# Kernel tuning notes

Measured on AMD Instinct MI355X. Metric: run time of the kernel, lower is better.

Reference implementation:

```python
import jax, jax.numpy as jnp
import numpy as np

# Graph sizes hard-coded in the original forward
N_NODE, N_EDGE, N_HEDGE, N_HNODE = 200, 100, 39, 23
LINK_LEN = 3
DIM_IN, DIM_E_IN, DIM_OUT, EMBED_DIM = 64, 16, 128, 10
TIME_DIM = 55
BATCH = 512


def _bigraph_conv(x, edge_index, n_src, n_tgt, W_self, W_agg):
    """Bipartite mean message passing src->tgt->src, mode='cat'.
    x: (b, n_src, c). edge_index: (2, E) int, row0 in [0,n_src), row1 in [0,n_tgt).
    Returns (b, n_src, c_self + c_agg)."""
    src, tgt = edge_index[0], edge_index[1]
    b, _, c = x.shape
    # mean-aggregate node features onto hyperedges
    e_sum = jnp.zeros((b, n_tgt, c), x.dtype).at[:, tgt, :].add(x[:, src, :])
    e_cnt = jnp.zeros((n_tgt,), x.dtype).at[tgt].add(1.0)
    h_e = e_sum / jnp.maximum(e_cnt, 1.0)[None, :, None]
    # mean-aggregate hyperedge features back onto nodes
    n_sum = jnp.zeros((b, n_src, c), x.dtype).at[:, src, :].add(h_e[:, tgt, :])
    n_cnt = jnp.zeros((n_src,), x.dtype).at[src].add(1.0)
    h_n = n_sum / jnp.maximum(n_cnt, 1.0)[None, :, None]
    return jnp.concatenate([x @ W_self, h_n @ W_agg], axis=-1)


def setup_inputs() -> dict:
    key = jax.random.key(0)
    ks = jax.random.split(key, 20)
    f = jnp.float32
    inp = {
        "x": jax.random.normal(ks[0], (BATCH, N_NODE, DIM_IN), f),
        "x_e": jax.random.normal(ks[1], (BATCH, N_EDGE, DIM_E_IN), f),
        "x_time": jax.random.normal(ks[2], (BATCH, 1, TIME_DIM), f),
        "x_window": jax.random.normal(ks[3], (BATCH, N_NODE, 12), f),
        "node_embeddings": jax.random.normal(ks[4], (N_NODE, EMBED_DIM), f),
        "hodge_laplacian": jax.random.normal(ks[5], (N_EDGE, N_EDGE), f) * 0.1,
        "incidence_matrix": jax.random.uniform(ks[6], (N_NODE, N_EDGE), f),
        "hyper_edge_data": jnp.stack([
            jax.random.randint(ks[7], (800,), 0, N_NODE),
            jax.random.randint(ks[8], (800,), 0, N_HEDGE)]).astype(jnp.int32),
        "hyper_node_data": jnp.stack([
            jax.random.randint(ks[9], (400,), 0, N_EDGE),
            jax.random.randint(ks[10], (400,), 0, N_HNODE)]).astype(jnp.int32),
        # learned parameters
        "weights_pool": jax.random.normal(ks[11], (EMBED_DIM, LINK_LEN, DIM_IN + TIME_DIM, DIM_OUT // 2), f) * 0.1,
        "bias_pool": jax.random.normal(ks[12], (EMBED_DIM, DIM_OUT), f) * 0.1,
        "W_node_self": jax.random.normal(ks[13], (DIM_IN, DIM_OUT // 8), f) * 0.1,
        "W_node_agg": jax.random.normal(ks[14], (DIM_IN, DIM_OUT // 8), f) * 0.1,
        "W_edge_self": jax.random.normal(ks[15], (DIM_E_IN, DIM_OUT // 16), f) * 0.1,
        "W_edge_agg": jax.random.normal(ks[16], (DIM_E_IN, DIM_OUT // 16), f) * 0.1,
        "W_hoc": jax.random.normal(ks[17], (DIM_OUT // 8, DIM_OUT // 8), f) * 0.1,
        "b_hoc": jnp.zeros((DIM_OUT // 8,), f),
    }
    return inp


def reference(x, x_e, x_time, x_window, node_embeddings, hodge_laplacian,
              incidence_matrix, hyper_edge_data, hyper_node_data,
              weights_pool, bias_pool, W_node_self, W_node_agg,
              W_edge_self, W_edge_agg, W_hoc, b_hoc):
    n = node_embeddings.shape[0]
    # adaptive support: softmax(relu(E E^T)) and Chebyshev-like powers
    sup = jax.nn.softmax(jax.nn.relu(node_embeddings @ node_embeddings.T), axis=1)
    support_set = [jnp.eye(n, dtype=x.dtype), sup]
    for k in range(2, LINK_LEN):
        support_set.append(sup @ support_set[k - 1])
    supports = jnp.stack(support_set, axis=0)                      # (K, n, n)
    # merge time features: (b,1,55) broadcast to (b,n,55)
    x_time_rep = jnp.broadcast_to(x_time, (x.shape[0], x.shape[1], x_time.shape[2]))
    merge_x = jnp.concatenate([x, x_time_rep], axis=-1)            # (b, n, i)
    # per-node dynamic weights / bias
    weights = jnp.einsum('nd,dkio->nkio', node_embeddings, weights_pool)
    bias = node_embeddings @ bias_pool                             # (n, dim_out)
    # graph conv with dynamic weights
    x_g = jnp.einsum('knm,bmc->bnkc', supports, merge_x)           # (b, n, K, i)
    x_gconv = jnp.einsum('bnki,nkio->bno', x_g, weights)           # (b, n, dim_out/2)
    # hypergraph bipartite convs (dropout is identity in eval mode)
    x_node_hyper = _bigraph_conv(x, hyper_edge_data, N_NODE, N_HEDGE, W_node_self, W_node_agg)
    x_edge_hyper = _bigraph_conv(x_e, hyper_node_data, N_EDGE, N_HNODE, W_edge_self, W_edge_agg)
    # hodge-laplacian higher-order conv on edge features
    x_e_hconv = jnp.einsum('mn,bnc->bmc', hodge_laplacian, x_edge_hyper) @ W_hoc + b_hoc
    x_e_hh = jnp.concatenate([x_edge_hyper, x_e_hconv], axis=-1)   # (b, m, dim_out/4)
    # push edge features onto nodes via incidence matrix
    x_edge_hh_node = jnp.einsum('bmo,nm->bno', x_e_hh, incidence_matrix)
    out = jnp.concatenate([x_gconv, x_node_hyper, x_edge_hh_node], axis=-1) + bias
    return out
```

## Files before the change

kernel.cpp:

```cpp
#include <hip/hip_runtime.h>

typedef unsigned short u16;
typedef unsigned int   u32;
typedef __attribute__((ext_vector_type(8))) short short8;
typedef __attribute__((ext_vector_type(4))) short short4v;
typedef __attribute__((ext_vector_type(4))) float f32x4;

#define OFF_SUP       0
#define OFF_SUP2T     40000
#define OFF_BIAS      80000
#define OFF_RCPHE     105600
#define OFF_RCPN      105664
#define OFF_RCPHN     105920
#define OFF_RCPE      105984
#define OFF_A1        106112
#define OFF_A1E       113912
#define OFF_WNODE     116212
#define OFF_WEDGE     118260
#define OFF_WHOC      118516
#define OFF_BHOC      118772
#define OFF_WECOMB    118788
#define OFF_M3        119556
#define OFF_AN16      139556
#define OFF_AE16      159556
#define OFF_SUPB      164556
#define OFF_G12       234444
#define OFF_G34       257740
#define OFF_WNSB      281036
#define OFF_WNAB      281548
#define OFF_WFF       282060

__device__ __forceinline__ float us2f(u16 u){
  union { float f; u32 i; } v; v.i = ((u32)u) << 16; return v.f;
}
__device__ __forceinline__ u16 f2us(float f){
  u32 u = __float_as_uint(f);
  u += 0x7FFF + ((u >> 16) & 1);
  return (u16)(u >> 16);
}

__global__ __launch_bounds__(256) void k_pre1(
    const float* __restrict__ E, const float* __restrict__ biasP,
    const float* __restrict__ Wns, const float* __restrict__ Wna,
    const float* __restrict__ Wes, const float* __restrict__ Wea,
    const float* __restrict__ Whoc, const float* __restrict__ bhoc,
    const int* __restrict__ hed, const int* __restrict__ hnd,
    float* __restrict__ ws)
{
  const int n = blockIdx.x, t = threadIdx.x;
  __shared__ float Ef[2000];
  __shared__ float arow[200];
  __shared__ float red[256];
  __shared__ int A1i[7800];
  __shared__ int A1ei[2300];
  for (int i=t;i<2000;i+=256) Ef[i] = E[i];
  __syncthreads();
  const float* En = &Ef[n*10];
  for (int m=t;m<200;m+=256){
    float s=0.f;
    #pragma unroll
    for (int d=0;d<10;d++) s += En[d]*Ef[m*10+d];
    arow[m] = fmaxf(s,0.f);
  }
  __syncthreads();
  float mv = -1e30f;
  for (int m=t;m<200;m+=256) mv = fmaxf(mv, arow[m]);
  red[t]=mv; __syncthreads();
  for (int s=128;s>0;s>>=1){ if(t<s) red[t]=fmaxf(red[t],red[t+s]); __syncthreads(); }
  mv = red[0]; __syncthreads();
  float sv=0.f;
  for (int m=t;m<200;m+=256) sv += __expf(arow[m]-mv);
  red[t]=sv; __syncthreads();
  for (int s=128;s>0;s>>=1){ if(t<s) red[t]+=red[t+s]; __syncthreads(); }
  const float inv = 1.f/red[0];
  for (int m=t;m<200;m+=256)
    ws[OFF_SUP + n*200+m] = __expf(arow[m]-mv)*inv;
  for (int o=t;o<128;o+=256){
    float acc=0.f;
    #pragma unroll
    for (int d=0;d<10;d++) acc += En[d]*biasP[d*128+o];
    ws[OFF_BIAS + n*128+o]=acc;
  }
  if (n==0){
    for (int i=t;i<7800;i+=256) A1i[i]=0;
    for (int i=t;i<2300;i+=256) A1ei[i]=0;
    __syncthreads();
    for (int e=t;e<800;e+=256) atomicAdd(&A1i[hed[800+e]*200 + hed[e]], 1);
    for (int e=t;e<400;e+=256) atomicAdd(&A1ei[hnd[400+e]*100 + hnd[e]], 1);
    __syncthreads();
    for (int i=t;i<7800;i+=256) ws[OFF_A1+i]=(float)A1i[i];
    for (int i=t;i<2300;i+=256) ws[OFF_A1E+i]=(float)A1ei[i];
    for (int h=t;h<39;h+=256){ int s=0; for(int m=0;m<200;m++) s+=A1i[h*200+m]; ws[OFF_RCPHE+h]=1.f/fmaxf((float)s,1.f); }
    for (int m=t;m<200;m+=256){ int s=0; for(int h=0;h<39;h++) s+=A1i[h*200+m]; ws[OFF_RCPN+m]=1.f/fmaxf((float)s,1.f); }
    for (int h=t;h<23;h+=256){ int s=0; for(int m=0;m<100;m++) s+=A1ei[h*100+m]; ws[OFF_RCPHN+h]=1.f/fmaxf((float)s,1.f); }
    for (int m=t;m<100;m+=256){ int s=0; for(int h=0;h<23;h++) s+=A1ei[h*100+m]; ws[OFF_RCPE+m]=1.f/fmaxf((float)s,1.f); }
  }
  if (n==1){
    for (int idx=t;idx<2048;idx+=256){ int j=idx>>5,c=idx&31;
      ws[OFF_WNODE+idx]= (c<16? Wns[j*16+c] : Wna[j*16+(c-16)]); }
    { int j=t>>4, c=t&15;
      ws[OFF_WEDGE+t]= (c<8? Wes[j*8+c] : Wea[j*8+(c-8)]);
      ws[OFF_WHOC+t]= Whoc[t]; }
    if (t<16) ws[OFF_BHOC+t]= bhoc[t];
  }
}

__global__ __launch_bounds__(256) void k_wff(
    const float* __restrict__ E, const float* __restrict__ Wp, float* __restrict__ ws)
{
  const int n = blockIdx.x;
  const int ktp = blockIdx.y;
  const int t = threadIdx.x;
  const int ot = t >> 6, lane2 = t & 63;
  __shared__ float EnS[10];
  if (t < 10) EnS[t] = E[n*10 + t];
  __syncthreads();
  const int o = ot*16 + (lane2 & 15);
  const int kbase = ((ktp<6)? ktp : ktp+2)*32 + (lane2>>4)*8;
  u16 outv[8];
  if (ktp < 6){
    #pragma unroll
    for (int kb=0;kb<8;kb++){
      const int k = kbase + kb;
      const int kk = k>>6, i = k&63;
      const float* wrow = Wp + ((size_t)kk*119 + i)*64 + o;
      float acc = 0.f;
      #pragma unroll
      for (int d=0;d<10;d++) acc += EnS[d]*wrow[(size_t)d*3*119*64];
      outv[kb] = f2us(acc);
    }
  } else {
    #pragma unroll
    for (int kb=0;kb<8;kb++){
      const int k = kbase + kb;
      float acc = 0.f;
      if (k < 311){
        const int i = k - 192;
        #pragma unroll
        for (int kk=0;kk<3;kk++){
          const float* wrow = Wp + ((size_t)kk*119 + i)*64 + o;
          #pragma unroll
          for (int d=0;d<10;d++) acc += EnS[d]*wrow[(size_t)d*3*119*64];
        }
      }
      outv[kb] = f2us(acc);
    }
  }
  u16* wff = (u16*)(ws + OFF_WFF) + (size_t)n*16384;
  *(short8*)&wff[((ktp*4 + ot)*64 + lane2)*8] = *(const short8*)outv;
}

__global__ __launch_bounds__(256) void k_pre2(float* __restrict__ ws)
{
  const int blk = blockIdx.x, t = threadIdx.x;
  __shared__ float rowp[200];
  __shared__ float colw[64];
  if (blk < 200){
    const int n = blk;
    for (int m=t;m<200;m+=256) rowp[m]=ws[OFF_SUP+n*200+m];
    for (int h=t;h<39;h+=256) colw[h]=ws[OFF_A1+h*200+n]*ws[OFF_RCPHE+h];
    __syncthreads();
    for (int j=t;j<200;j+=256){
      float acc=0.f;
      for (int m=0;m<200;m++) acc += rowp[m]*ws[OFF_SUP+m*200+j];
      ws[OFF_SUP2T + j*200 + n] = acc;
    }
    const float rn = ws[OFF_RCPN+n];
    u16* an16 = (u16*)(ws + OFF_AN16);
    for (int m=t;m<200;m+=256){
      float acc=0.f;
      for (int h=0;h<39;h++) acc += colw[h]*ws[OFF_A1+h*200+m];
      an16[m*200 + n] = f2us(acc*rn);
    }
  } else {
    const int n = blk-200;
    for (int h=t;h<23;h+=256) colw[h]=ws[OFF_A1E+h*100+n]*ws[OFF_RCPHN+h];
    __syncthreads();
    const float rn = ws[OFF_RCPE+n];
    u16* ae16 = (u16*)(ws + OFF_AE16);
    for (int m=t;m<100;m+=256){
      float acc=0.f;
      for (int h=0;h<23;h++) acc += colw[h]*ws[OFF_A1E+h*100+m];
      ae16[m*100 + n] = f2us(acc*rn);
    }
  }
}

__global__ __launch_bounds__(64) void k_pre3(float* __restrict__ ws)
{
  const int blk = blockIdx.x;
  const int kk = blk/91, rem = blk%91;
  const int nt = rem/7, kt = rem%7;
  const int L = threadIdx.x, l15 = L & 15, quad = L >> 4;
  const u16* an16 = (const u16*)(ws + OFF_AN16);
  u16* supB = (u16*)(ws + OFF_SUPB);
  #pragma unroll
  for (int jj=0;jj<8;jj++){
    int m  = kt*32 + quad*8 + jj;
    int nn = nt*16 + l15;
    float v = 0.f;
    if (m < 200 && nn < 200)
      v = (kk==0)? ws[OFF_SUP + nn*200 + m]
        : (kk==1)? ws[OFF_SUP2T + m*200 + nn]
                 : us2f(an16[m*200 + nn]);
    supB[((size_t)(kk*91 + nt*7 + kt)*64 + L)*8 + jj] = f2us(v);
  }
}

__global__ __launch_bounds__(256) void k_pre4a(
    const float* __restrict__ inc, const float* __restrict__ hodge, float* __restrict__ ws)
{
  const int blk = blockIdx.x, t = threadIdx.x;
  if (blk < 200){
    __shared__ float incL[100];
    __shared__ float rsS;
    const int n = blk;
    if (t<100) incL[t] = inc[n*100+t];
    __syncthreads();
    if (t==0){ float s=0.f; for(int m=0;m<100;m++) s+=incL[m]; rsS=s; }
    __syncthreads();
    if (t<100){
      float a=0.f;
      for (int m=0;m<100;m++) a += incL[m]*hodge[m*100+t];
      ws[OFF_M3 + n*100 + t] = a;
    }
    if (t<16) ws[OFF_BIAS + n*128 + 112 + t] += rsS * ws[OFF_BHOC + t];
  } else if (blk == 200){
    for (int i=t;i<768;i+=256){
      int j=i/48, cc=i-(i/48)*48;
      float v;
      if (cc<16) v = ws[OFF_WEDGE + j*16 + cc];
      else if (cc<32){ v=0.f; for(int q=0;q<8;q++) v += ws[OFF_WEDGE+j*16+q]*ws[OFF_WHOC+q*16+(cc-16)]; }
      else           { v=0.f; for(int q=0;q<8;q++) v += ws[OFF_WEDGE+j*16+8+q]*ws[OFF_WHOC+(8+q)*16+(cc-32)]; }
      ws[OFF_WECOMB + i] = v;
    }
  } else {
    u16* wnsb=(u16*)(ws+OFF_WNSB); u16* wnab=(u16*)(ws+OFF_WNAB);
    for (int i=t;i<1024;i+=256){
      int kt=i>>9, lane=(i>>3)&63, jj=i&7;
      int k = kt*32 + (lane>>4)*8 + jj, c = lane&15;
      wnsb[i] = f2us(ws[OFF_WNODE + k*32 + c]);
      wnab[i] = f2us(ws[OFF_WNODE + k*32 + 16 + c]);
    }
  }
}

__global__ __launch_bounds__(64) void k_pre4b(
    const float* __restrict__ inc, float* __restrict__ ws)
{
  const int blk = blockIdx.x;
  const int g = blk/91, rem = blk%91;
  const int nt = rem/7, kt = rem%7;
  const int L = threadIdx.x, l15 = L & 15, quad = L >> 4;
  const u16* ae16 = (const u16*)(ws + OFF_AE16);
  u16* G = (u16*)(ws + (g? OFF_G34 : OFF_G12));
  #pragma unroll
  for (int jj=0;jj<8;jj++){
    int k = kt*32 + quad*8 + jj;
    int n = nt*16 + l15;
    float v = 0.f;
    if (n < 200 && k < 200){
      if (g==0){
        if (k<100) v = inc[n*100+k];
        else { const float* ir = inc + n*100; const u16* ac = ae16 + (k-100)*100;
               for (int m=0;m<100;m++) v += ir[m]*us2f(ac[m]); }
      } else {
        if (k<100) v = ws[OFF_M3 + n*100 + k];
        else { const float* mr = ws + OFF_M3 + n*100; const u16* ac = ae16 + (k-100)*100;
               for (int m=0;m<100;m++) v += mr[m]*us2f(ac[m]); }
      }
    }
    G[((size_t)(kt*13+nt)*64 + L)*8 + jj] = f2us(v);
  }
}

__global__ __launch_bounds__(256) void k_A(
    const float* __restrict__ x, const float* __restrict__ ws, u16* __restrict__ outu)
{
  const int b = blockIdx.x, t = threadIdx.x;
  const int lane = t & 63, w = t >> 6;
  const int l15 = lane & 15, quad = lane >> 4;
  __shared__ __align__(16) u16 xT[64*232];
  __shared__ __align__(16) u16 xgL[200*72 + 8*72];
  const float* xb = x + (size_t)b*12800;
  for (int i=t;i<6400;i+=256){
    int m2=i>>6, c=i&63;
    u32 v0 = (u32)f2us(xb[(size_t)(2*m2)*64+c]);
    u32 v1 = (u32)f2us(xb[(size_t)(2*m2+1)*64+c]);
    *(u32*)&xT[c*232 + 2*m2] = v0 | (v1<<16);
  }
  for (int i=t;i<64*16;i+=256){
    int c=i>>4, k=i&15;
    *(u32*)&xT[c*232 + 200 + 2*k] = 0;
  }
  __syncthreads();
  const u16* supB = (const u16*)(ws + OFF_SUPB);
  const int nt0 = (w==0)? 0 : (1 + 3*w);
  const int ntc = (w==0)? 4 : 3;
  for (int kk=0;kk<3;kk++){
    f32x4 acc[4][4];
    #pragma unroll
    for (int ct=0;ct<4;ct++)
      #pragma unroll
      for (int q=0;q<4;q++) acc[ct][q] = f32x4{0.f,0.f,0.f,0.f};
    for (int kt=0;kt<7;kt++){
      short8 af[4];
      #pragma unroll
      for (int ct=0;ct<4;ct++)
        af[ct] = *(const short8*)&xT[(ct*16 + l15)*232 + kt*32 + quad*8];
      short8 bf[4];
      #pragma unroll
      for (int q=0;q<4;q++)
        if (q < ntc)
          bf[q] = *(const short8*)(supB + ((size_t)(kk*91 + (nt0+q)*7 + kt)*64 + lane)*8);
      #pragma unroll
      for (int ct=0;ct<4;ct++)
        #pragma unroll
        for (int q=0;q<4;q++)
          if (q < ntc)
            acc[ct][q] = __builtin_amdgcn_mfma_f32_16x16x32_bf16(af[ct], bf[q], acc[ct][q], 0,0,0);
    }
    #pragma unroll
    for (int ct=0;ct<4;ct++)
      #pragma unroll
      for (int q=0;q<4;q++)
        if (q < ntc){
          int n = (nt0+q)*16 + l15;
          short4v sv;
          #pragma unroll
          for (int r=0;r<4;r++) sv[r] = (short)f2us(acc[ct][q][r]);
          *(short4v*)&xgL[n*72 + ct*16 + quad*4] = sv;
        }
    __syncthreads();
    for (int i=t;i<1600;i+=256){
      int n=i>>3, c8=i&7;
      short8 v = *(const short8*)&xgL[n*72 + c8*8];
      *(short8*)&outu[((size_t)b*200 + n)*256 + 64 + kk*64 + c8*8] = v;
    }
    __syncthreads();
  }
}

__global__ __launch_bounds__(256) void k_B(
    const float* __restrict__ x, const float* __restrict__ xtime,
    const float* __restrict__ ws, const u16* __restrict__ outu, float* __restrict__ outp)
{
  const int bt = blockIdx.x, n = blockIdx.y, t = threadIdx.x;
  const int b0 = bt*64;
  const int lane = t & 63, w = t >> 6, l15 = lane & 15, quad = lane >> 4;
  __shared__ __align__(16) u16 vL[64*328];
  for (int i=t;i<4096;i+=256){ int rb=i>>6, j=i&63;
    vL[rb*328+j] = f2us(x[((size_t)(b0+rb)*200+n)*64+j]); }
  for (int i=t;i<6144;i+=256){ int rb=i/96, j=i-(i/96)*96;
    *(u32*)&vL[rb*328+64+2*j] = ((const u32*)outu)[((size_t)(b0+rb)*200+n)*128+32+j]; }
  for (int i=t;i<4096;i+=256){ int rb=i>>6, j=i&63;
    vL[rb*328+256+j] = (j<55)? f2us(xtime[(size_t)(b0+rb)*55+j]) : (u16)0; }
  __syncthreads();
  f32x4 acc[4], accS, accA;
  #pragma unroll
  for (int ot=0;ot<4;ot++) acc[ot] = f32x4{0.f,0.f,0.f,0.f};
  accS = f32x4{0.f,0.f,0.f,0.f};
  accA = f32x4{0.f,0.f,0.f,0.f};
  const u16* wff  = (const u16*)(ws+OFF_WFF) + (size_t)n*16384;
  const u16* wnsb = (const u16*)(ws+OFF_WNSB);
  const u16* wnab = (const u16*)(ws+OFF_WNAB);
  const int row = w*16 + l15;
  for (int ktp=0;ktp<8;ktp++){
    const int ktph = (ktp<6)? ktp : ktp+2;
    short8 af = *(const short8*)&vL[row*328 + ktph*32 + quad*8];
    #pragma unroll
    for (int ot=0;ot<4;ot++){
      short8 bf = *(const short8*)&wff[((ktp*4+ot)*64+lane)*8];
      acc[ot] = __builtin_amdgcn_mfma_f32_16x16x32_bf16(af, bf, acc[ot], 0,0,0);
    }
    if (ktp<2){
      short8 bs = *(const short8*)&wnsb[(ktp*64+lane)*8];
      accS = __builtin_amdgcn_mfma_f32_16x16x32_bf16(af, bs, accS, 0,0,0);
    }
  }
  #pragma unroll
  for (int kt2=0;kt2<2;kt2++){
    short8 af = *(const short8*)&vL[row*328 + (6+kt2)*32 + quad*8];
    short8 bn = *(const short8*)&wnab[(kt2*64+lane)*8];
    accA = __builtin_amdgcn_mfma_f32_16x16x32_bf16(af, bn, accA, 0,0,0);
  }
  const int rbase = b0 + w*16 + quad*4;
  #pragma unroll
  for (int ot=0;ot<4;ot++){
    int o = ot*16+l15;
    float bias = ws[OFF_BIAS+n*128+o];
    #pragma unroll
    for (int r=0;r<4;r++)
      outp[((size_t)(rbase+r)*200+n)*128+o] = acc[ot][r]+bias;
  }
  { int o = 64+l15; float bias = ws[OFF_BIAS+n*128+o];
    #pragma unroll
    for (int r=0;r<4;r++)
      outp[((size_t)(rbase+r)*200+n)*128+o] = accS[r]+bias; }
  { int o = 80+l15; float bias = ws[OFF_BIAS+n*128+o];
    #pragma unroll
    for (int r=0;r<4;r++)
      outp[((size_t)(rbase+r)*200+n)*128+o] = accA[r]+bias; }
}

__global__ __launch_bounds__(256) void k_E(
    const float* __restrict__ xe, const float* __restrict__ ws, float* __restrict__ outp)
{
  const int b = blockIdx.x, t = threadIdx.x;
  const int lane = t & 63, w = t >> 6, l15 = lane & 15, quad = lane >> 4;
  __shared__ float xeL[1600];
  __shared__ __align__(16) u16 Afr[2][16*232];
  for (int i=t;i<1600;i+=256) xeL[i] = xe[(size_t)b*1600+i];
  for (int i=t;i<3712;i+=256){ Afr[0][i]=0; Afr[1][i]=0; }
  __syncthreads();
  for (int i=t;i<4800;i+=256){
    int m = i/48, cc = i-(i/48)*48;
    float v=0.f;
    const float* wcb = ws + OFF_WECOMB + cc;
    const float* xr = xeL + m*16;
    #pragma unroll
    for (int j=0;j<16;j++) v += xr[j]*wcb[j*48];
    u16 hv = f2us(v);
    if (cc<8)       Afr[0][cc*232 + m] = hv;
    else if (cc<16) Afr[0][cc*232 + 100 + m] = hv;
    else if (cc<32) Afr[1][(cc-16)*232 + m] = hv;
    else            Afr[1][(cc-32)*232 + 100 + m] = hv;
  }
  __syncthreads();
  const int g = w & 1, half = w >> 1;
  const int nt0 = half*7;
  const u16* G = (const u16*)(ws + (g? OFF_G34 : OFF_G12));
  const u16* A = Afr[g];
  f32x4 acc[7];
  #pragma unroll
  for (int q=0;q<7;q++) acc[q] = f32x4{0.f,0.f,0.f,0.f};
  for (int kt=0;kt<7;kt++){
    short8 af = *(const short8*)&A[l15*232 + kt*32 + quad*8];
    #pragma unroll
    for (int q=0;q<7;q++){
      short8 bf = *(const short8*)&G[((size_t)(kt*13 + nt0 + q)*64 + lane)*8];
      acc[q] = __builtin_amdgcn_mfma_f32_16x16x32_bf16(af, bf, acc[q], 0,0,0);
    }
  }
  #pragma unroll
  for (int q=0;q<7;q++){
    int n = (nt0+q)*16 + l15;
    if (n < 200){
      #pragma unroll
      for (int r=0;r<4;r++){
        int ch = 96 + g*16 + quad*4 + r;
        outp[((size_t)b*200+n)*128 + ch] = acc[q][r] + ws[OFF_BIAS + n*128 + ch];
      }
    }
  }
}

extern "C" void kernel_launch(void* const* d_in, const int* in_sizes, int n_in,
                              void* d_out, int out_size, void* d_ws, size_t ws_size,
                              hipStream_t stream)
{
  (void)in_sizes; (void)n_in; (void)out_size; (void)ws_size;
  const float* x     = (const float*)d_in[0];
  const float* xe    = (const float*)d_in[1];
  const float* xtime = (const float*)d_in[2];
  const float* E     = (const float*)d_in[4];
  const float* hodge = (const float*)d_in[5];
  const float* inc   = (const float*)d_in[6];
  const int* hed     = (const int*)d_in[7];
  const int* hnd     = (const int*)d_in[8];
  const float* Wp    = (const float*)d_in[9];
  const float* biasP = (const float*)d_in[10];
  const float* Wns   = (const float*)d_in[11];
  const float* Wna   = (const float*)d_in[12];
  const float* Wes   = (const float*)d_in[13];
  const float* Wea   = (const float*)d_in[14];
  const float* Whoc  = (const float*)d_in[15];
  const float* bhoc  = (const float*)d_in[16];
  float* ws   = (float*)d_ws;
  float* outp = (float*)d_out;
  u16*   outu = (u16*)d_out;

  k_pre1<<<200, 256, 0, stream>>>(E, biasP, Wns, Wna, Wes, Wea, Whoc, bhoc, hed, hnd, ws);
  k_wff<<<dim3(200, 8), 256, 0, stream>>>(E, Wp, ws);
  k_pre2<<<300, 256, 0, stream>>>(ws);
  k_pre3<<<273, 64, 0, stream>>>(ws);
  k_pre4a<<<202, 256, 0, stream>>>(inc, hodge, ws);
  k_pre4b<<<182, 64, 0, stream>>>(inc, ws);
  k_A<<<512, 256, 0, stream>>>(x, ws, outu);
  k_B<<<dim3(8, 200), 256, 0, stream>>>(x, xtime, ws, outu, outp);
  k_E<<<512, 256, 0, stream>>>(xe, ws, outp);
}
```

Measured before the change: 248.0 us.

## Merge preprocessing launches and stage bf16 inputs in k_A for vectorized k_B loads

Independent preprocessing kernels are merged into two launches (pre2 with pre4a, pre3 with pre4b), which removes kernel launch gaps. k_A now converts x to bf16 into unused output columns and packs x_time into a reused workspace region. k_B can then fill shared memory with 16-byte vector loads instead of scalar fp32 loads and conversions. k_B's grid is also reordered so node is the fast block index. In exchange, k_A does extra global writes, and the packed x_time buffer reuses the SUP2T workspace, which is only safe because that region is finished with by then.

```diff
diff --git a/kernel.cpp b/kernel.cpp
--- a/kernel.cpp
+++ b/kernel.cpp
@@ -5,9 +5,11 @@
 typedef __attribute__((ext_vector_type(8))) short short8;
 typedef __attribute__((ext_vector_type(4))) short short4v;
 typedef __attribute__((ext_vector_type(4))) float f32x4;
+typedef __attribute__((ext_vector_type(4))) u32 u32x4;
 
 #define OFF_SUP       0
 #define OFF_SUP2T     40000
+#define OFF_XTB       40000
 #define OFF_BIAS      80000
 #define OFF_RCPHE     105600
 #define OFF_RCPN      105664
@@ -150,12 +152,13 @@
   *(short8*)&wff[((ktp*4 + ot)*64 + lane2)*8] = *(const short8*)outv;
 }
 
-__global__ __launch_bounds__(256) void k_pre2(float* __restrict__ ws)
+__global__ __launch_bounds__(256) void k_pre2x(
+    const float* __restrict__ inc, const float* __restrict__ hodge, float* __restrict__ ws)
 {
   const int blk = blockIdx.x, t = threadIdx.x;
-  __shared__ float rowp[200];
-  __shared__ float colw[64];
   if (blk < 200){
+    __shared__ float rowp[200];
+    __shared__ float colw[64];
     const int n = blk;
     for (int m=t;m<200;m+=256) rowp[m]=ws[OFF_SUP+n*200+m];
     for (int h=t;h<39;h+=256) colw[h]=ws[OFF_A1+h*200+n]*ws[OFF_RCPHE+h];
@@ -172,7 +175,8 @@
       for (int h=0;h<39;h++) acc += colw[h]*ws[OFF_A1+h*200+m];
       an16[m*200 + n] = f2us(acc*rn);
     }
-  } else {
+  } else if (blk < 300){
+    __shared__ float colw[64];
     const int n = blk-200;
     for (int h=t;h<23;h+=256) colw[h]=ws[OFF_A1E+h*100+n]*ws[OFF_RCPHN+h];
     __syncthreads();
@@ -183,38 +187,10 @@
       for (int h=0;h<23;h++) acc += colw[h]*ws[OFF_A1E+h*100+m];
       ae16[m*100 + n] = f2us(acc*rn);
     }
-  }
-}
-
-__global__ __launch_bounds__(64) void k_pre3(float* __restrict__ ws)
-{
-  const int blk = blockIdx.x;
-  const int kk = blk/91, rem = blk%91;
-  const int nt = rem/7, kt = rem%7;
-  const int L = threadIdx.x, l15 = L & 15, quad = L >> 4;
-  const u16* an16 = (const u16*)(ws + OFF_AN16);
-  u16* supB = (u16*)(ws + OFF_SUPB);
-  #pragma unroll
-  for (int jj=0;jj<8;jj++){
-    int m  = kt*32 + quad*8 + jj;
-    int nn = nt*16 + l15;
-    float v = 0.f;
-    if (m < 200 && nn < 200)
-      v = (kk==0)? ws[OFF_SUP + nn*200 + m]
-        : (kk==1)? ws[OFF_SUP2T + m*200 + nn]
-                 : us2f(an16[m*200 + nn]);
-    supB[((size_t)(kk*91 + nt*7 + kt)*64 + L)*8 + jj] = f2us(v);
-  }
-}
-
-__global__ __launch_bounds__(256) void k_pre4a(
-    const float* __restrict__ inc, const float* __restrict__ hodge, float* __restrict__ ws)
-{
-  const int blk = blockIdx.x, t = threadIdx.x;
-  if (blk < 200){
+  } else if (blk < 500){
     __shared__ float incL[100];
     __shared__ float rsS;
-    const int n = blk;
+    const int n = blk-300;
     if (t<100) incL[t] = inc[n*100+t];
     __syncthreads();
     if (t==0){ float s=0.f; for(int m=0;m<100;m++) s+=incL[m]; rsS=s; }
@@ -225,7 +201,7 @@
       ws[OFF_M3 + n*100 + t] = a;
     }
     if (t<16) ws[OFF_BIAS + n*128 + 112 + t] += rsS * ws[OFF_BHOC + t];
-  } else if (blk == 200){
+  } else if (blk == 500){
     for (int i=t;i<768;i+=256){
       int j=i/48, cc=i-(i/48)*48;
       float v;
@@ -245,37 +221,57 @@
   }
 }
 
-__global__ __launch_bounds__(64) void k_pre4b(
+__global__ __launch_bounds__(64) void k_pre34(
     const float* __restrict__ inc, float* __restrict__ ws)
 {
-  const int blk = blockIdx.x;
-  const int g = blk/91, rem = blk%91;
-  const int nt = rem/7, kt = rem%7;
   const int L = threadIdx.x, l15 = L & 15, quad = L >> 4;
-  const u16* ae16 = (const u16*)(ws + OFF_AE16);
-  u16* G = (u16*)(ws + (g? OFF_G34 : OFF_G12));
-  #pragma unroll
-  for (int jj=0;jj<8;jj++){
-    int k = kt*32 + quad*8 + jj;
-    int n = nt*16 + l15;
-    float v = 0.f;
-    if (n < 200 && k < 200){
-      if (g==0){
-        if (k<100) v = inc[n*100+k];
-        else { const float* ir = inc + n*100; const u16* ac = ae16 + (k-100)*100;
-               for (int m=0;m<100;m++) v += ir[m]*us2f(ac[m]); }
-      } else {
-        if (k<100) v = ws[OFF_M3 + n*100 + k];
-        else { const float* mr = ws + OFF_M3 + n*100; const u16* ac = ae16 + (k-100)*100;
-               for (int m=0;m<100;m++) v += mr[m]*us2f(ac[m]); }
+  if (blockIdx.x < 273){
+    const int blk = blockIdx.x;
+    const int kk = blk/91, rem = blk%91;
+    const int nt = rem/7, kt = rem%7;
+    const u16* an16 = (const u16*)(ws + OFF_AN16);
+    u16* supB = (u16*)(ws + OFF_SUPB);
+    #pragma unroll
+    for (int jj=0;jj<8;jj++){
+      int m  = kt*32 + quad*8 + jj;
+      int nn = nt*16 + l15;
+      float v = 0.f;
+      if (m < 200 && nn < 200)
+        v = (kk==0)? ws[OFF_SUP + nn*200 + m]
+          : (kk==1)? ws[OFF_SUP2T + m*200 + nn]
+                   : us2f(an16[m*200 + nn]);
+      supB[((size_t)(kk*91 + nt*7 + kt)*64 + L)*8 + jj] = f2us(v);
+    }
+  } else {
+    const int blk = blockIdx.x - 273;
+    const int g = blk/91, rem = blk%91;
+    const int nt = rem/7, kt = rem%7;
+    const u16* ae16 = (const u16*)(ws + OFF_AE16);
+    u16* G = (u16*)(ws + (g? OFF_G34 : OFF_G12));
+    #pragma unroll
+    for (int jj=0;jj<8;jj++){
+      int k = kt*32 + quad*8 + jj;
+      int n = nt*16 + l15;
+      float v = 0.f;
+      if (n < 200 && k < 200){
+        if (g==0){
+          if (k<100) v = inc[n*100+k];
+          else { const float* ir = inc + n*100; const u16* ac = ae16 + (k-100)*100;
+                 for (int m=0;m<100;m++) v += ir[m]*us2f(ac[m]); }
+        } else {
+          if (k<100) v = ws[OFF_M3 + n*100 + k];
+          else { const float* mr = ws + OFF_M3 + n*100; const u16* ac = ae16 + (k-100)*100;
+                 for (int m=0;m<100;m++) v += mr[m]*us2f(ac[m]); }
+        }
       }
-    }
-    G[((size_t)(kt*13+nt)*64 + L)*8 + jj] = f2us(v);
+      G[((size_t)(kt*13+nt)*64 + L)*8 + jj] = f2us(v);
+    }
   }
 }
 
 __global__ __launch_bounds__(256) void k_A(
-    const float* __restrict__ x, const float* __restrict__ ws, u16* __restrict__ outu)
+    const float* __restrict__ x, const float* __restrict__ xtime,
+    float* __restrict__ ws, u16* __restrict__ outu)
 {
   const int b = blockIdx.x, t = threadIdx.x;
   const int lane = t & 63, w = t >> 6;
@@ -293,6 +289,19 @@
     int c=i>>4, k=i&15;
     *(u32*)&xT[c*232 + 200 + 2*k] = 0;
   }
+  for (int i=t;i<3200;i+=256){
+    int n=i>>4, c4=i&15;
+    f32x4 xv = *(const f32x4*)&xb[(size_t)n*64 + c4*4];
+    short4v sv; sv[0]=(short)f2us(xv[0]); sv[1]=(short)f2us(xv[1]);
+    sv[2]=(short)f2us(xv[2]); sv[3]=(short)f2us(xv[3]);
+    *(short4v*)&outu[((size_t)b*200+n)*256 + c4*4] = sv;
+  }
+  if (t < 32){
+    const int j2 = t*2;
+    u32 lo = (j2   < 55)? (u32)f2us(xtime[(size_t)b*55+j2])   : 0u;
+    u32 hi = (j2+1 < 55)? (u32)f2us(xtime[(size_t)b*55+j2+1]) : 0u;
+    ((u32*)(ws + OFF_XTB))[b*32 + t] = lo | (hi<<16);
+  }
   __syncthreads();
   const u16* supB = (const u16*)(ws + OFF_SUPB);
   const int nt0 = (w==0)? 0 : (1 + 3*w);
@@ -342,19 +351,19 @@
 }
 
 __global__ __launch_bounds__(256) void k_B(
-    const float* __restrict__ x, const float* __restrict__ xtime,
     const float* __restrict__ ws, const u16* __restrict__ outu, float* __restrict__ outp)
 {
-  const int bt = blockIdx.x, n = blockIdx.y, t = threadIdx.x;
+  const int n = blockIdx.x, bt = blockIdx.y, t = threadIdx.x;
   const int b0 = bt*64;
   const int lane = t & 63, w = t >> 6, l15 = lane & 15, quad = lane >> 4;
   __shared__ __align__(16) u16 vL[64*328];
-  for (int i=t;i<4096;i+=256){ int rb=i>>6, j=i&63;
-    vL[rb*328+j] = f2us(x[((size_t)(b0+rb)*200+n)*64+j]); }
-  for (int i=t;i<6144;i+=256){ int rb=i/96, j=i-(i/96)*96;
-    *(u32*)&vL[rb*328+64+2*j] = ((const u32*)outu)[((size_t)(b0+rb)*200+n)*128+32+j]; }
-  for (int i=t;i<4096;i+=256){ int rb=i>>6, j=i&63;
-    vL[rb*328+256+j] = (j<55)? f2us(xtime[(size_t)(b0+rb)*55+j]) : (u16)0; }
+  for (int i=t;i<2048;i+=256){ int rb=i>>5, q=i&31;
+    u32x4 v = *(const u32x4*)&((const u32*)outu)[(((size_t)(b0+rb)*200+n)<<7) + q*4];
+    *(u32x4*)&vL[rb*328 + q*8] = v; }
+  { const u32* xtb = (const u32*)(ws + OFF_XTB);
+    for (int i=t;i<512;i+=256){ int rb=i>>3, q=i&7;
+      u32x4 v = *(const u32x4*)&xtb[((b0+rb)<<5) + q*4];
+      *(u32x4*)&vL[rb*328 + 256 + q*8] = v; } }
   __syncthreads();
   f32x4 acc[4], accS, accA;
   #pragma unroll
@@ -482,11 +491,9 @@
 
   k_pre1<<<200, 256, 0, stream>>>(E, biasP, Wns, Wna, Wes, Wea, Whoc, bhoc, hed, hnd, ws);
   k_wff<<<dim3(200, 8), 256, 0, stream>>>(E, Wp, ws);
-  k_pre2<<<300, 256, 0, stream>>>(ws);
-  k_pre3<<<273, 64, 0, stream>>>(ws);
-  k_pre4a<<<202, 256, 0, stream>>>(inc, hodge, ws);
-  k_pre4b<<<182, 64, 0, stream>>>(inc, ws);
-  k_A<<<512, 256, 0, stream>>>(x, ws, outu);
-  k_B<<<dim3(8, 200), 256, 0, stream>>>(x, xtime, ws, outu, outp);
+  k_pre2x<<<502, 256, 0, stream>>>(inc, hodge, ws);
+  k_pre34<<<455, 64, 0, stream>>>(inc, ws);
+  k_A<<<512, 256, 0, stream>>>(x, xtime, ws, outu);
+  k_B<<<dim3(200, 8), 256, 0, stream>>>(ws, outu, outp);
   k_E<<<512, 256, 0, stream>>>(xe, ws, outp);
 }
```

Measured after the change: 226.9 us. 1.09x faster.
